# Performance work log

Measured on AMD Instinct MI355X. Metric: run time of the kernel, lower is better.

## Reference

```python
import jax, jax.numpy as jnp
import numpy as np

# Faithful math of CustomAttn(method='tanh').forward:
#   E[i,j] = Linear_{4h->1}( tanh( concat(e_i, e_j) ) )
#          = w[:2h] . tanh(e_i) + w[2h:] . tanh(e_j) + b
#   out    = softmax(E, axis=0)
# Since tanh is elementwise and the linear layer is a dot product, the
# pairwise score decomposes into a_i + b_j + bias, computed with two
# O(n*d) matvecs and one broadcasted add (honoring the original math
# exactly while avoiding the O(n^2) python loop).

SEQ_LEN = 8192
HIDDEN = 256  # hidden_size; feature dim of encoder_outputs is 2*HIDDEN


def setup_inputs() -> dict:
    key = jax.random.key(0)
    k1, k2 = jax.random.split(key)
    encoder_outputs = jax.random.normal(k1, (SEQ_LEN, 2 * HIDDEN), dtype=jnp.float32)
    attn2_w = jax.random.normal(k2, (4 * HIDDEN,), dtype=jnp.float32) * (1.0 / np.sqrt(4 * HIDDEN))
    attn2_b = jnp.zeros((1,), dtype=jnp.float32)
    return {"encoder_outputs": encoder_outputs, "attn2_w": attn2_w, "attn2_b": attn2_b}


def reference(encoder_outputs, attn2_w, attn2_b):
    d = encoder_outputs.shape[1]  # 2*hidden_size
    t = jnp.tanh(encoder_outputs)            # [S, 2h]
    a = t @ attn2_w[:d]                      # [S], contribution of e_i
    b = t @ attn2_w[d:]                      # [S], contribution of e_j
    energies = a[:, None] + b[None, :] + attn2_b[0]  # [S, S]
    return jax.nn.softmax(energies, axis=0)
```

## Files before the change

kernel.cpp:

```cpp
#include <hip/hip_runtime.h>
#include <math.h>

#define SEQ 8192
#define DIM 512

__global__ __launch_bounds__(256) void ca_compute_a(
    const float* __restrict__ e, const float* __restrict__ w,
    float* __restrict__ a) {
    const int wave = threadIdx.x >> 6;
    const int lane = threadIdx.x & 63;
    const int row  = blockIdx.x * 4 + wave;
    const float* er = e + (size_t)row * DIM + lane * 8;
    const float* wr = w + lane * 8;

    float4 e0 = *reinterpret_cast<const float4*>(er);
    float4 e1 = *reinterpret_cast<const float4*>(er + 4);
    float4 w0 = *reinterpret_cast<const float4*>(wr);
    float4 w1 = *reinterpret_cast<const float4*>(wr + 4);

    float sum = tanhf(e0.x) * w0.x + tanhf(e0.y) * w0.y +
                tanhf(e0.z) * w0.z + tanhf(e0.w) * w0.w +
                tanhf(e1.x) * w1.x + tanhf(e1.y) * w1.y +
                tanhf(e1.z) * w1.z + tanhf(e1.w) * w1.w;

    #pragma unroll
    for (int off = 32; off; off >>= 1) sum += __shfl_down(sum, off, 64);
    if (lane == 0) a[row] = sum;
}

__global__ __launch_bounds__(1024) void ca_softmax(
    const float* __restrict__ a, float* __restrict__ p) {
    __shared__ float red[16];
    __shared__ float bcast;
    const int tid = threadIdx.x;

    float vals[8];
    float m = -INFINITY;
    #pragma unroll
    for (int k = 0; k < 8; ++k) {
        vals[k] = a[tid + k * 1024];
        m = fmaxf(m, vals[k]);
    }
    #pragma unroll
    for (int off = 32; off; off >>= 1) m = fmaxf(m, __shfl_down(m, off, 64));
    if ((tid & 63) == 0) red[tid >> 6] = m;
    __syncthreads();
    if (tid == 0) {
        float v = red[0];
        #pragma unroll
        for (int i = 1; i < 16; ++i) v = fmaxf(v, red[i]);
        bcast = v;
    }
    __syncthreads();
    m = bcast;

    float s = 0.f;
    #pragma unroll
    for (int k = 0; k < 8; ++k) {
        vals[k] = expf(vals[k] - m);
        s += vals[k];
    }
    __syncthreads();
    #pragma unroll
    for (int off = 32; off; off >>= 1) s += __shfl_down(s, off, 64);
    if ((tid & 63) == 0) red[tid >> 6] = s;
    __syncthreads();
    if (tid == 0) {
        float v = 0.f;
        #pragma unroll
        for (int i = 0; i < 16; ++i) v += red[i];
        bcast = v;
    }
    __syncthreads();
    const float inv = 1.0f / bcast;
    #pragma unroll
    for (int k = 0; k < 8; ++k) p[tid + k * 1024] = vals[k] * inv;
}

__global__ __launch_bounds__(256) void ca_broadcast(
    const float* __restrict__ p, float4* __restrict__ out) {
    const int row = blockIdx.x;
    const float v = p[row];
    const float4 f = make_float4(v, v, v, v);
    float4* o = out + (size_t)row * (SEQ / 4);
    #pragma unroll
    for (int k = 0; k < (SEQ / 4) / 256; ++k)
        o[threadIdx.x + k * 256] = f;
}

extern "C" void kernel_launch(void* const* d_in, const int* in_sizes, int n_in,
                              void* d_out, int out_size, void* d_ws, size_t ws_size,
                              hipStream_t stream) {
    const float* enc = (const float*)d_in[0];
    const float* w   = (const float*)d_in[1];
    float* out = (float*)d_out;

    float* a = (float*)d_ws;
    float* p = a + SEQ;

    ca_compute_a<<<SEQ / 4, 256, 0, stream>>>(enc, w, a);
    ca_softmax<<<1, 1024, 0, stream>>>(a, p);
    ca_broadcast<<<SEQ, 256, 0, stream>>>(p, (float4*)out);
}
```

Baseline: 56.16 us.

## Fuse softmax normalization into broadcast kernel and drop max subtraction

Computes exp(a) directly in the first kernel, skipping the max pass, and merges the single-block softmax with the output broadcast. Each of the 2048 broadcast blocks now redundantly reduces the 8192-element exp vector to get the normalizer, then writes four rows with nontemporal stores. This removes one launch and the serial single-block softmax stage, at the cost of redundant reductions per block and possible overflow because the max is no longer subtracted.

```diff
diff --git a/kernel.cpp b/kernel.cpp
--- a/kernel.cpp
+++ b/kernel.cpp
@@ -4,9 +4,11 @@
 #define SEQ 8192
 #define DIM 512
 
-__global__ __launch_bounds__(256) void ca_compute_a(
+typedef float floatx4 __attribute__((ext_vector_type(4)));
+
+__global__ __launch_bounds__(256) void ca_exp_a(
     const float* __restrict__ e, const float* __restrict__ w,
-    float* __restrict__ a) {
+    float* __restrict__ exp_a) {
     const int wave = threadIdx.x >> 6;
     const int lane = threadIdx.x & 63;
     const int row  = blockIdx.x * 4 + wave;
@@ -25,67 +27,38 @@
 
     #pragma unroll
     for (int off = 32; off; off >>= 1) sum += __shfl_down(sum, off, 64);
-    if (lane == 0) a[row] = sum;
+    if (lane == 0) exp_a[row] = expf(sum);
 }
 
-__global__ __launch_bounds__(1024) void ca_softmax(
-    const float* __restrict__ a, float* __restrict__ p) {
+__global__ __launch_bounds__(1024) void ca_norm_bcast(
+    const float* __restrict__ exp_a, floatx4* __restrict__ out) {
     __shared__ float red[16];
-    __shared__ float bcast;
     const int tid = threadIdx.x;
 
-    float vals[8];
-    float m = -INFINITY;
-    #pragma unroll
-    for (int k = 0; k < 8; ++k) {
-        vals[k] = a[tid + k * 1024];
-        m = fmaxf(m, vals[k]);
-    }
-    #pragma unroll
-    for (int off = 32; off; off >>= 1) m = fmaxf(m, __shfl_down(m, off, 64));
-    if ((tid & 63) == 0) red[tid >> 6] = m;
-    __syncthreads();
-    if (tid == 0) {
-        float v = red[0];
-        #pragma unroll
-        for (int i = 1; i < 16; ++i) v = fmaxf(v, red[i]);
-        bcast = v;
-    }
-    __syncthreads();
-    m = bcast;
-
-    float s = 0.f;
-    #pragma unroll
-    for (int k = 0; k < 8; ++k) {
-        vals[k] = expf(vals[k] - m);
-        s += vals[k];
-    }
-    __syncthreads();
+    const floatx4* ev = reinterpret_cast<const floatx4*>(exp_a);
+    floatx4 v0 = ev[tid * 2];
+    floatx4 v1 = ev[tid * 2 + 1];
+    float s = ((v0.x + v0.y) + (v0.z + v0.w)) +
+              ((v1.x + v1.y) + (v1.z + v1.w));
     #pragma unroll
     for (int off = 32; off; off >>= 1) s += __shfl_down(s, off, 64);
     if ((tid & 63) == 0) red[tid >> 6] = s;
     __syncthreads();
-    if (tid == 0) {
-        float v = 0.f;
-        #pragma unroll
-        for (int i = 0; i < 16; ++i) v += red[i];
-        bcast = v;
-    }
-    __syncthreads();
-    const float inv = 1.0f / bcast;
+    float S = 0.f;
     #pragma unroll
-    for (int k = 0; k < 8; ++k) p[tid + k * 1024] = vals[k] * inv;
-}
+    for (int i = 0; i < 16; ++i) S += red[i];
+    const float inv = 1.0f / S;
 
-__global__ __launch_bounds__(256) void ca_broadcast(
-    const float* __restrict__ p, float4* __restrict__ out) {
-    const int row = blockIdx.x;
-    const float v = p[row];
-    const float4 f = make_float4(v, v, v, v);
-    float4* o = out + (size_t)row * (SEQ / 4);
+    const int sub = tid >> 8;
+    const int t   = tid & 255;
+    const int row = blockIdx.x * 4 + sub;
+    const float p = exp_a[row] * inv;
+    floatx4 f;
+    f.x = p; f.y = p; f.z = p; f.w = p;
+    floatx4* o = out + (size_t)row * (SEQ / 4) + t;
     #pragma unroll
-    for (int k = 0; k < (SEQ / 4) / 256; ++k)
-        o[threadIdx.x + k * 256] = f;
+    for (int k = 0; k < 8; ++k)
+        __builtin_nontemporal_store(f, o + k * 256);
 }
 
 extern "C" void kernel_launch(void* const* d_in, const int* in_sizes, int n_in,
@@ -95,10 +68,8 @@
     const float* w   = (const float*)d_in[1];
     float* out = (float*)d_out;
 
-    float* a = (float*)d_ws;
-    float* p = a + SEQ;
+    float* exp_a = (float*)d_ws;
 
-    ca_compute_a<<<SEQ / 4, 256, 0, stream>>>(enc, w, a);
-    ca_softmax<<<1, 1024, 0, stream>>>(a, p);
-    ca_broadcast<<<SEQ, 256, 0, stream>>>(p, (float4*)out);
+    ca_exp_a<<<SEQ / 4, 256, 0, stream>>>(enc, w, exp_a);
+    ca_norm_bcast<<<SEQ / 4, 1024, 0, stream>>>(exp_a, (floatx4*)out);
 }
```

Result: slower. 60.10 us (+7.0%).
